# Optimization experiments

Hardware: AMD Instinct MI355X
Metric: run time of the kernel (lower is better)

## Reference

```python
import jax, jax.numpy as jnp
import numpy as np
from jax import lax

DN = ('NCHW', 'OIHW', 'NCHW')

def conv(x, w, b):
    y = lax.conv_general_dilated(x, w, (1, 1), 'SAME', dimension_numbers=DN)
    return y + b[None, :, None, None]


def setup_inputs() -> dict:
    key = jax.random.key(0)
    ks = jax.random.split(key, 32)
    B, C, H, W = 16, 256, 40, 100
    dim, N, kd, ncls, mdim = 134, 4, 128, 2, 256
    inc = C + 2
    s = 0.05  # weight init scale
    def w(k, shape):
        return jax.random.normal(k, shape, jnp.float32) * s
    d = {}
    d['features'] = jax.random.normal(ks[0], (B, C, H, W), jnp.float32)
    d['iw0'] = w(ks[1], (dim, inc, 3, 3)); d['ib0'] = jnp.zeros((dim,), jnp.float32)
    d['iw1'] = w(ks[2], (dim, dim, 3, 3)); d['ib1'] = jnp.zeros((dim,), jnp.float32)
    d['iw2'] = w(ks[3], (dim, dim, 3, 3)); d['ib2'] = jnp.zeros((dim,), jnp.float32)
    d['iw3'] = w(ks[4], (dim, dim, 3, 3)); d['ib3'] = jnp.zeros((dim,), jnp.float32)
    d['iam_w'] = w(ks[5], (N, dim, 3, 3)); d['iam_b'] = jnp.zeros((N,), jnp.float32)
    d['cls_w'] = w(ks[6], (ncls, dim));    d['cls_b'] = jnp.zeros((ncls,), jnp.float32)
    d['mk_w'] = w(ks[7], (kd, dim));       d['mk_b'] = jnp.zeros((kd,), jnp.float32)
    d['mw0'] = w(ks[8], (mdim, inc, 3, 3));  d['mb0'] = jnp.zeros((mdim,), jnp.float32)
    d['mw1'] = w(ks[9], (mdim, mdim, 3, 3)); d['mb1'] = jnp.zeros((mdim,), jnp.float32)
    d['mw2'] = w(ks[10], (mdim, mdim, 3, 3)); d['mb2'] = jnp.zeros((mdim,), jnp.float32)
    d['mw3'] = w(ks[11], (mdim, mdim, 3, 3)); d['mb3'] = jnp.zeros((mdim,), jnp.float32)
    d['pw'] = w(ks[12], (kd, mdim, 1, 1));   d['pb'] = jnp.zeros((kd,), jnp.float32)
    return d


def reference(features, iw0, ib0, iw1, ib1, iw2, ib2, iw3, ib3, iam_w, iam_b,
              cls_w, cls_b, mk_w, mk_b, mw0, mb0, mw1, mb1, mw2, mb2, mw3, mb3, pw, pb):
    B, C, H, W = features.shape
    # coordinate channels in [-1, 1]
    y_loc = -1.0 + 2.0 * jnp.arange(H, dtype=jnp.float32) / (H - 1)
    x_loc = -1.0 + 2.0 * jnp.arange(W, dtype=jnp.float32) / (W - 1)
    yy, xx = jnp.meshgrid(y_loc, x_loc, indexing='ij')  # [H,W]
    coords = jnp.broadcast_to(jnp.stack([xx, yy], 0)[None], (B, 2, H, W))
    feat = jnp.concatenate([coords, features], axis=1)  # [B, C+2, H, W]

    # instance branch conv stack (258 -> 134, relu)
    f = jax.nn.relu(conv(feat, iw0, ib0))
    f = jax.nn.relu(conv(f, iw1, ib1))
    f = jax.nn.relu(conv(f, iw2, ib2))
    f = jax.nn.relu(conv(f, iw3, ib3))  # [B,134,H,W]

    params = jnp.transpose(f, (0, 2, 3, 1)).reshape(-1, 134)  # [B*H*W, 134]

    iam = conv(f, iam_w, iam_b)           # [B,N,H,W]
    iam_prob = jax.nn.sigmoid(iam)
    Bn, Ni = iam_prob.shape[:2]

    # seed extraction: per-map flat argmax (pos = r*W + c, label always 0 in original)
    pos = jnp.argmax(iam_prob.reshape(Bn * Ni, H * W), axis=-1)  # [B*N], values in [0, H*W)
    sel = params[pos]                     # gather rows (indexes batch-0 region, as in source)
    mask_params = sel[:, :67]
    reg_params = sel[:, 67:]

    # iam-weighted pooling
    ip = iam_prob.reshape(Bn, Ni, H * W)
    ip = ip / jnp.clip(ip.sum(-1, keepdims=True), 1e-6)
    inst = jnp.einsum('bnl,bcl->bnc', ip, f.reshape(Bn, 134, H * W))  # [B,N,134]

    pred_logits = inst @ cls_w.T + cls_b  # [B,N,2]
    pred_kernel = inst @ mk_w.T + mk_b    # [B,N,128]

    # mask branch (258 -> 256 x4 relu, then 1x1 projection to 128, no relu)
    m = jax.nn.relu(conv(feat, mw0, mb0))
    m = jax.nn.relu(conv(m, mw1, mb1))
    m = jax.nn.relu(conv(m, mw2, mb2))
    m = jax.nn.relu(conv(m, mw3, mb3))
    mf = conv(m, pw, pb)                  # [B,128,H,W]

    pred_masks = jnp.einsum('bnk,bkl->bnl', pred_kernel, mf.reshape(Bn, 128, H * W))
    pred_masks = pred_masks.reshape(Bn * Ni, H, W)
    pred_logits = pred_logits.reshape(Bn * Ni, -1)
    return pred_logits, mask_params, reg_params, pred_masks
```

## Files before the change

### kernel.cpp

```cpp
#include <hip/hip_runtime.h>
#include <hip/hip_bf16.h>
#include <math.h>

constexpr int HW = 4000;
constexpr int HP = 4284;
constexpr int HPAD = 4480;
constexpr int NPIXH = 16 * HP;

typedef short s16x8 __attribute__((ext_vector_type(8)));
typedef float f32x4 __attribute__((ext_vector_type(4)));
typedef unsigned short u16x4 __attribute__((ext_vector_type(4)));
typedef unsigned short u16;

__device__ __forceinline__ u16 f2bf(float f) {
    __hip_bfloat16 h = __float2bfloat16(f);
    u16 b; __builtin_memcpy(&b, &h, 2); return b;
}
__device__ __forceinline__ float bf2f(u16 b) {
    __hip_bfloat16 h; __builtin_memcpy(&h, &b, 2); return __bfloat162float(h);
}

__device__ __forceinline__ void gload_lds16(const void* g, void* l) {
    __builtin_amdgcn_global_load_lds(
        (const __attribute__((address_space(1))) void*)g,
        (__attribute__((address_space(3))) void*)l, 16, 0, 0);
}

__global__ __launch_bounds__(256) void repack_w(
    const float* __restrict__ W, u16* __restrict__ Wh, u16* __restrict__ Wl,
    int Cout, int Cin, int NRS, int nCh, int Npad, int do_lo)
{
    const int chunk = blockIdx.x * 256 + threadIdx.x;
    const int per = Npad * 4;
    const int total = NRS * nCh * per;
    if (chunk >= total) return;
    const int q = chunk % per;
    const int t2 = chunk / per;
    const int ch = t2 % nCh;
    const int rs = t2 / nCh;
    const int f = q >> 6, g = (q >> 4) & 3, rA = q & 15;
    const int n = f * 16 + rA;
    u16x4 hp[2], lp[2];
    #pragma unroll
    for (int j = 0; j < 8; ++j) {
        const int c = ch * 32 + g * 8 + j;
        const float v = (n < Cout && c < Cin) ? W[((size_t)n * Cin + c) * NRS + rs] : 0.f;
        const u16 hb = f2bf(v);
        hp[j >> 2][j & 3] = hb;
        lp[j >> 2][j & 3] = f2bf(v - bf2f(hb));
    }
    const size_t o = (size_t)chunk * 8;
    *(u16x4*)(Wh + o) = hp[0]; *(u16x4*)(Wh + o + 4) = hp[1];
    if (do_lo) { *(u16x4*)(Wl + o) = lp[0]; *(u16x4*)(Wl + o + 4) = lp[1]; }
}

__global__ __launch_bounds__(256) void prep_x0(
    const float* __restrict__ feat, u16* __restrict__ Xh, u16* __restrict__ Xl)
{
    const int p = blockIdx.x * 256 + threadIdx.x;
    if (p >= NPIXH) return;
    const int b = p / HP; const int rem = p - b * HP;
    const int hh = rem / 102, wp = rem - hh * 102;
    const bool halo = (hh == 0) | (hh == 41) | (wp == 0) | (wp == 101);
    const int h = hh - 1, w = wp - 1;
    const int hw = h * 100 + w;
    const float xw = -1.f + 2.f * (float)w / 99.f;
    const float yh = -1.f + 2.f * (float)h / 39.f;
    for (int g = 0; g < 36; ++g) {
        u16x4 hp[2], lp[2];
        #pragma unroll
        for (int j = 0; j < 8; ++j) {
            const int c = g * 8 + j;
            float v = 0.f;
            if (!halo) {
                if (c == 0) v = xw;
                else if (c == 1) v = yh;
                else if (c < 258) v = feat[((size_t)(b * 256 + (c - 2))) * HW + hw];
            }
            const u16 hb = f2bf(v);
            hp[j >> 2][j & 3] = hb;
            lp[j >> 2][j & 3] = f2bf(v - bf2f(hb));
        }
        const size_t o = ((size_t)(b * 36 + g) * HPAD + rem) * 8;
        *(u16x4*)(Xh + o) = hp[0]; *(u16x4*)(Xh + o + 4) = hp[1];
        *(u16x4*)(Xl + o) = lp[0]; *(u16x4*)(Xl + o + 4) = lp[1];
    }
}

__global__ __launch_bounds__(256) void zero_halo_pl(
    u16* __restrict__ pa, u16* __restrict__ pb, int nGa, int nGb)
{
    const int p = blockIdx.x * 256 + threadIdx.x;
    if (p >= NPIXH) return;
    const int b = p / HP; const int rem = p - b * HP;
    const int hh = rem / 102, wp = rem - hh * 102;
    if (!((hh == 0) | (hh == 41) | (wp == 0) | (wp == 101))) return;
    const u16x4 z = {0, 0, 0, 0};
    for (int g = 0; g < nGa; ++g) {
        const size_t o = ((size_t)(b * nGa + g) * HPAD + rem) * 8;
        *(u16x4*)(pa + o) = z; *(u16x4*)(pa + o + 4) = z;
    }
    if (pb)
        for (int g = 0; g < nGb; ++g) {
            const size_t o = ((size_t)(b * nGb + g) * HPAD + rem) * 8;
            *(u16x4*)(pb + o) = z; *(u16x4*)(pb + o + 4) = z;
        }
}

template <int SPLIT, int BN, int NRS, int OUTMODE, int NCH>
__global__ __launch_bounds__(256, 2) void conv_mfma(
    const u16* __restrict__ Xhi, const u16* __restrict__ Xlo,
    const u16* __restrict__ Whi, const u16* __restrict__ Wlo,
    const float* __restrict__ bias,
    u16* __restrict__ Yhi, u16* __restrict__ Ylo, float* __restrict__ Yf,
    int Npad, int Cout, int CoutStore, int nGout, int do_relu,
    int nN, int cpx)
{
    constexpr int FW = BN / 32;
    constexpr int PSTRIDE = 393;
    constexpr int NGIN = NCH * 4;

    __shared__ u16 lsXh[4 * PSTRIDE * 8];
    __shared__ u16 lsXl[SPLIT == 3 ? 4 * PSTRIDE * 8 : 8];

    const int tid = threadIdx.x, lane = tid & 63, wid = tid >> 6;

    const int pb_ = blockIdx.x;
    const int s = (pb_ & 7) * cpx + (pb_ >> 3);
    const int nb = s % nN;
    const int mt = s / nN;
    const int mb = mt & 31, bimg = mt >> 5;
    const int off = mb * 128;
    const int n0 = nb * BN;
    const int h0 = off / 100, w0 = off - h0 * 100;
    const int pTL0 = h0 * 102 + w0;

    const int wn = (wid & 1) * (BN / 2);
    const int wm = (wid >> 1) * 64;
    const int gA = lane >> 4, rA = lane & 15;
    const int wq0 = ((n0 + wn) >> 4) * 64;

    int pd[4]; bool mval[4];
    #pragma unroll
    for (int fb = 0; fb < 4; ++fb) {
        int mm = off + wm + fb * 16 + rA;
        mval[fb] = mm < HW;
        if (!mval[fb]) mm = HW - 1;
        const int h = mm / 100, w = mm - h * 100;
        pd[fb] = (h * 102 + w) - pTL0;
    }

    auto stageX = [&](int ch) {
        const size_t src = ((size_t)(bimg * NGIN + ch * 4 + wid) * HPAD + pTL0) * 8;
        char* dst = (char*)lsXh + wid * (PSTRIDE * 16);
        char* dstl = (char*)lsXl + wid * (PSTRIDE * 16);
        #pragma unroll
        for (int i = 0; i < 6; ++i) {
            gload_lds16(Xhi + src + (size_t)(i * 64 + lane) * 8, dst + i * 1024);
            if constexpr (SPLIT == 3)
                gload_lds16(Xlo + src + (size_t)(i * 64 + lane) * 8, dstl + i * 1024);
        }
    };

    s16x8 wh[2][FW];
    s16x8 wl[2][SPLIT == 3 ? FW : 1];
    auto loadW = [&](int ch, int rs, int buf) {
        const size_t base = (((size_t)rs * NCH + ch) * (Npad * 4) + wq0 + lane) * 8;
        #pragma unroll
        for (int fa = 0; fa < FW; ++fa) {
            wh[buf][fa] = *(const s16x8*)(Whi + base + fa * 64 * 8);
            if constexpr (SPLIT == 3)
                wl[buf][fa] = *(const s16x8*)(Wlo + base + fa * 64 * 8);
        }
    };

    f32x4 acc[FW][4];
    #pragma unroll
    for (int i = 0; i < FW; ++i)
        #pragma unroll
        for (int j = 0; j < 4; ++j) acc[i][j] = (f32x4){0.f, 0.f, 0.f, 0.f};

    #pragma unroll 1
    for (int ch = 0; ch < NCH; ++ch) {
        if (ch) __syncthreads();
        stageX(ch);
        loadW(ch, 0, 0);
        __syncthreads();

        #pragma unroll
        for (int rs = 0; rs < NRS; ++rs) {
            if (rs + 1 < NRS) loadW(ch, rs + 1, (rs + 1) & 1);
            const int toff = (NRS == 9) ? ((rs / 3) * 102 + (rs % 3)) : 103;

            s16x8 bX[4], bXl[SPLIT == 3 ? 4 : 1];
            #pragma unroll
            for (int fb = 0; fb < 4; ++fb) {
                const int xi = (gA * PSTRIDE + pd[fb] + toff) * 8;
                bX[fb] = *(const s16x8*)&lsXh[xi];
                if constexpr (SPLIT == 3) bXl[fb] = *(const s16x8*)&lsXl[xi];
            }
            #pragma unroll
            for (int fa = 0; fa < FW; ++fa)
                #pragma unroll
                for (int fb = 0; fb < 4; ++fb) {
                    acc[fa][fb] = __builtin_amdgcn_mfma_f32_16x16x32_bf16(
                        wh[rs & 1][fa], bX[fb], acc[fa][fb], 0, 0, 0);
                    if constexpr (SPLIT == 3) {
                        acc[fa][fb] = __builtin_amdgcn_mfma_f32_16x16x32_bf16(
                            wh[rs & 1][fa], bXl[fb], acc[fa][fb], 0, 0, 0);
                        acc[fa][fb] = __builtin_amdgcn_mfma_f32_16x16x32_bf16(
                            wl[rs & 1][fa], bX[fb], acc[fa][fb], 0, 0, 0);
                    }
                }
        }
    }

    #pragma unroll
    for (int fb = 0; fb < 4; ++fb) {
        if (!mval[fb]) continue;
        const int mm = off + wm + fb * 16 + rA;
        #pragma unroll
        for (int fa = 0; fa < FW; ++fa) {
            const int nbc = n0 + wn + fa * 16 + gA * 4;
            if (nbc >= CoutStore) continue;
            f32x4 v = acc[fa][fb];
            #pragma unroll
            for (int i = 0; i < 4; ++i) {
                const int n = nbc + i;
                float x = (n < Cout) ? (v[i] + bias[n]) : 0.f;
                if (do_relu) x = fmaxf(x, 0.f);
                v[i] = x;
            }
            if constexpr (OUTMODE == 2) {
                *(f32x4*)(Yf + (size_t)(bimg * HW + mm) * CoutStore + nbc) = v;
            } else {
                const size_t o =
                    ((size_t)(bimg * nGout + (nbc >> 3)) * HPAD + pTL0 + pd[fb] + 103) * 8 + (nbc & 7);
                u16x4 hp;
                #pragma unroll
                for (int i = 0; i < 4; ++i) hp[i] = f2bf(v[i]);
                *(u16x4*)(Yhi + o) = hp;
                if constexpr (OUTMODE == 0) {
                    u16x4 lp;
                    #pragma unroll
                    for (int i = 0; i < 4; ++i) lp[i] = f2bf(v[i] - bf2f(hp[i]));
                    *(u16x4*)(Ylo + o) = lp;
                }
            }
        }
    }
}

__global__ __launch_bounds__(256) void iam_conv_nhwc(
    const u16* __restrict__ fhi, const u16* __restrict__ flo,
    const float* __restrict__ Wt, const float* __restrict__ bias,
    float* __restrict__ iam)
{
    __shared__ float wsm[9 * 134 * 4];
    const int tid = threadIdx.x;
    for (int i = tid; i < 4824; i += 256) {
        const int rs = i / 536; const int rem = i - rs * 536;
        const int c = rem >> 2; const int n = rem & 3;
        wsm[i] = Wt[(n * 134 + c) * 9 + rs];
    }
    __syncthreads();
    const int m = blockIdx.x * 256 + tid;
    const int b = m / HW; const int hw = m - b * HW;
    const int h = hw / 100, w = hw - h * 100;
    const int pTL = h * 102 + w;
    float a0 = bias[0], a1 = bias[1], a2 = bias[2], a3 = bias[3];
    for (int rs = 0; rs < 9; ++rs) {
        const int pA = pTL + (rs / 3) * 102 + (rs % 3);
        const float* wrow = &wsm[rs * 536];
        for (int g = 0; g < 17; ++g) {
            const size_t o = ((size_t)(b * 20 + g) * HPAD + pA) * 8;
            s16x8 hv = *(const s16x8*)(fhi + o);
            s16x8 lv = *(const s16x8*)(flo + o);
            #pragma unroll
            for (int j = 0; j < 8; ++j) {
                const int c = g * 8 + j;
                if (c < 134) {
                    const float v = bf2f((u16)hv[j]) + bf2f((u16)lv[j]);
                    const float* wc = wrow + c * 4;
                    a0 = fmaf(v, wc[0], a0); a1 = fmaf(v, wc[1], a1);
                    a2 = fmaf(v, wc[2], a2); a3 = fmaf(v, wc[3], a3);
                }
            }
        }
    }
    iam[(b * 4 + 0) * HW + hw] = a0;
    iam[(b * 4 + 1) * HW + hw] = a1;
    iam[(b * 4 + 2) * HW + hw] = a2;
    iam[(b * 4 + 3) * HW + hw] = a3;
}

__device__ __forceinline__ float sigmoidf_dev(float x) {
    return 1.f / (1.f + expf(-x));
}

__global__ __launch_bounds__(256) void stats_kernel(
    const float* __restrict__ iam, int* __restrict__ pos, float* __restrict__ denom)
{
    const int i = blockIdx.x;
    const int tid = threadIdx.x;
    const float* p = &iam[i * HW];
    float bm = -1e30f; int bi = 0; float sum = 0.f;
    for (int l = tid; l < HW; l += 256) {
        const float s = sigmoidf_dev(p[l]);
        sum += s;
        if (s > bm) { bm = s; bi = l; }
    }
    __shared__ float sm[256]; __shared__ int si[256]; __shared__ float ss[256];
    sm[tid] = bm; si[tid] = bi; ss[tid] = sum;
    __syncthreads();
    for (int off = 128; off > 0; off >>= 1) {
        if (tid < off) {
            ss[tid] += ss[tid + off];
            const float m2 = sm[tid + off]; const int i2 = si[tid + off];
            if (m2 > sm[tid] || (m2 == sm[tid] && i2 < si[tid])) { sm[tid] = m2; si[tid] = i2; }
        }
        __syncthreads();
    }
    if (tid == 0) { pos[i] = si[0]; denom[i] = fmaxf(ss[0], 1e-6f); }
}

__global__ __launch_bounds__(256) void inst_nhwc(
    const u16* __restrict__ fhi, const u16* __restrict__ flo,
    const float* __restrict__ iam, const float* __restrict__ denom,
    float* __restrict__ inst)
{
    const int b = blockIdx.x, g = blockIdx.y;
    const int tid = threadIdx.x;
    float acc[4][8] = {};
    const size_t pbase = (size_t)(b * 20 + g) * HPAD;
    for (int l = tid; l < HW; l += 256) {
        const int p = (l / 100 + 1) * 102 + (l % 100) + 1;
        s16x8 hv = *(const s16x8*)(fhi + (pbase + p) * 8);
        s16x8 lv = *(const s16x8*)(flo + (pbase + p) * 8);
        float fv[8];
        #pragma unroll
        for (int j = 0; j < 8; ++j) fv[j] = bf2f((u16)hv[j]) + bf2f((u16)lv[j]);
        #pragma unroll
        for (int n = 0; n < 4; ++n) {
            const float s = sigmoidf_dev(iam[(b * 4 + n) * HW + l]);
            #pragma unroll
            for (int j = 0; j < 8; ++j) acc[n][j] = fmaf(s, fv[j], acc[n][j]);
        }
    }
    __shared__ float red[128];
    const int lane = tid & 63, wid = tid >> 6;
    #pragma unroll
    for (int n = 0; n < 4; ++n)
        #pragma unroll
        for (int j = 0; j < 8; ++j) {
            float v = acc[n][j];
            #pragma unroll
            for (int off = 32; off > 0; off >>= 1) v += __shfl_xor(v, off);
            if (lane == 0) red[wid * 32 + n * 8 + j] = v;
        }
    __syncthreads();
    if (tid < 32) {
        const float s = red[tid] + red[32 + tid] + red[64 + tid] + red[96 + tid];
        const int n = tid >> 3, j = tid & 7;
        const int c = g * 8 + j;
        if (c < 134) inst[(b * 4 + n) * 134 + c] = s / denom[b * 4 + n];
    }
}

__global__ __launch_bounds__(128) void head_kernel(
    const float* __restrict__ inst,
    const float* __restrict__ cls_w, const float* __restrict__ cls_b,
    const float* __restrict__ mk_w, const float* __restrict__ mk_b,
    float* __restrict__ out_logits, float* __restrict__ pk)
{
    const int i = blockIdx.x;
    const int tid = threadIdx.x;
    __shared__ float iv[134];
    for (int c = tid; c < 134; c += 128) iv[c] = inst[i * 134 + c];
    __syncthreads();
    float a = mk_b[tid];
    for (int c = 0; c < 134; ++c) a = fmaf(iv[c], mk_w[tid * 134 + c], a);
    pk[i * 128 + tid] = a;
    if (tid < 2) {
        float g = cls_b[tid];
        for (int c = 0; c < 134; ++c) g = fmaf(iv[c], cls_w[tid * 134 + c], g);
        out_logits[i * 2 + tid] = g;
    }
}

__global__ void gather_nhwc(
    const u16* __restrict__ fhi, const u16* __restrict__ flo,
    const int* __restrict__ pos, float* __restrict__ outm, float* __restrict__ outr)
{
    const int i = blockIdx.x;
    const int c = threadIdx.x;
    if (c >= 134) return;
    const int p = pos[i];
    const int ph = (p / 100 + 1) * 102 + (p % 100) + 1;
    const size_t o = ((size_t)(c >> 3) * HPAD + ph) * 8 + (c & 7);
    const float v = bf2f(fhi[o]) + bf2f(flo[o]);
    if (c < 67) outm[i * 67 + c] = v;
    else        outr[i * 67 + (c - 67)] = v;
}

__global__ __launch_bounds__(256) void maskout_nhwc(
    const float* __restrict__ pk, const float* __restrict__ mf,
    float* __restrict__ outm)
{
    const int b = blockIdx.x, lc = blockIdx.y;
    const int tid = threadIdx.x;
    __shared__ float pks[4][128];
    for (int i = tid; i < 512; i += 256) pks[i >> 7][i & 127] = pk[b * 512 + i];
    __syncthreads();
    const int l = lc * 256 + tid;
    if (l >= HW) return;
    const float* row = mf + (size_t)(b * HW + l) * 128;
    float a[4] = {};
    for (int k = 0; k < 128; k += 4) {
        const f32x4 mv = *(const f32x4*)(row + k);
        #pragma unroll
        for (int n = 0; n < 4; ++n) {
            a[n] = fmaf(pks[n][k + 0], mv[0], a[n]);
            a[n] = fmaf(pks[n][k + 1], mv[1], a[n]);
            a[n] = fmaf(pks[n][k + 2], mv[2], a[n]);
            a[n] = fmaf(pks[n][k + 3], mv[3], a[n]);
        }
    }
    #pragma unroll
    for (int n = 0; n < 4; ++n) outm[(b * 4 + n) * HW + l] = a[n];
}

extern "C" void kernel_launch(void* const* d_in, const int* in_sizes, int n_in,
                              void* d_out, int out_size, void* d_ws, size_t ws_size,
                              hipStream_t stream)
{
    const float* features = (const float*)d_in[0];
    const float* iw0 = (const float*)d_in[1];
    const float* ib0 = (const float*)d_in[2];
    const float* iw1 = (const float*)d_in[3];
    const float* ib1 = (const float*)d_in[4];
    const float* iw2 = (const float*)d_in[5];
    const float* ib2 = (const float*)d_in[6];
    const float* iw3 = (const float*)d_in[7];
    const float* ib3 = (const float*)d_in[8];
    const float* iam_w = (const float*)d_in[9];
    const float* iam_b = (const float*)d_in[10];
    const float* cls_w = (const float*)d_in[11];
    const float* cls_b = (const float*)d_in[12];
    const float* mk_w = (const float*)d_in[13];
    const float* mk_b = (const float*)d_in[14];
    const float* mw0 = (const float*)d_in[15];
    const float* mb0 = (const float*)d_in[16];
    const float* mw1 = (const float*)d_in[17];
    const float* mb1 = (const float*)d_in[18];
    const float* mw2 = (const float*)d_in[19];
    const float* mb2 = (const float*)d_in[20];
    const float* mw3 = (const float*)d_in[21];
    const float* mb3 = (const float*)d_in[22];
    const float* pw = (const float*)d_in[23];
    const float* pb = (const float*)d_in[24];

    constexpr size_t WI0 = (size_t)9 * 9 * 160 * 4 * 16;
    constexpr size_t WI123 = (size_t)9 * 5 * 160 * 4 * 16;
    constexpr size_t WM0 = (size_t)9 * 9 * 256 * 4 * 16;
    constexpr size_t WM123 = (size_t)9 * 8 * 256 * 4 * 16;
    constexpr size_t WPJ = (size_t)1 * 8 * 128 * 4 * 16;
    constexpr size_t PLANE = (size_t)HPAD * 16;
    constexpr size_t X0SZ = (size_t)16 * 36 * PLANE;
    constexpr size_t P20 = (size_t)16 * 20 * PLANE;

    char* ws = (char*)d_ws;
    size_t off = 0;
    auto carve = [&](size_t bytes) { char* p = ws + off; off += (bytes + 255) & ~(size_t)255; return p; };
    u16* wi0h = (u16*)carve(WI0); u16* wi0l = (u16*)carve(WI0);
    u16* wi1h = (u16*)carve(WI123); u16* wi1l = (u16*)carve(WI123);
    u16* wi2h = (u16*)carve(WI123); u16* wi2l = (u16*)carve(WI123);
    u16* wi3h = (u16*)carve(WI123); u16* wi3l = (u16*)carve(WI123);
    u16* wm0h = (u16*)carve(WM0);
    u16* wm1h = (u16*)carve(WM123); u16* wm2h = (u16*)carve(WM123); u16* wm3h = (u16*)carve(WM123);
    u16* wpjh = (u16*)carve(WPJ);
    u16* X0hi = (u16*)carve(X0SZ);
    char* RGA = carve(X0SZ);
    char* RGB = carve(2 * P20);
    char* RGC = carve(2 * P20);
    float* iamb = (float*)carve(1024000);
    int* pos = (int*)carve(256);
    float* denom = (float*)carve(256);
    float* instb = (float*)carve(34560);
    float* pkbuf = (float*)carve(32768);

    u16* X0lo = (u16*)RGA;
    u16* MBhi = (u16*)RGA;
    u16* RAhi = (u16*)RGB; u16* RAlo = (u16*)(RGB + P20);
    u16* MAhi = (u16*)RGB;
    u16* RBhi = (u16*)RGC; u16* RBlo = (u16*)(RGC + P20);
    float* mf = (float*)RGC;

    float* out_logits = (float*)d_out;
    float* out_mask = out_logits + 128;
    float* out_reg = out_mask + 64 * 67;
    float* out_masks = out_reg + 64 * 67;

    const dim3 blk(256);
    auto rp = [&](const float* W, u16* h, u16* l, int Cout_, int Cin_, int NRS_,
                  int nCh_, int Npad_, int dolo) {
        const int tot = NRS_ * nCh_ * Npad_ * 4;
        repack_w<<<dim3((tot + 255) / 256), blk, 0, stream>>>(W, h, l, Cout_, Cin_, NRS_, nCh_, Npad_, dolo);
    };
    rp(iw0, wi0h, wi0l, 134, 258, 9, 9, 160, 1);
    rp(iw1, wi1h, wi1l, 134, 134, 9, 5, 160, 1);
    rp(iw2, wi2h, wi2l, 134, 134, 9, 5, 160, 1);
    rp(iw3, wi3h, wi3l, 134, 134, 9, 5, 160, 1);
    rp(mw0, wm0h, nullptr, 256, 258, 9, 9, 256, 0);
    rp(mw1, wm1h, nullptr, 256, 256, 9, 8, 256, 0);
    rp(mw2, wm2h, nullptr, 256, 256, 9, 8, 256, 0);
    rp(mw3, wm3h, nullptr, 256, 256, 9, 8, 256, 0);
    rp(pw, wpjh, nullptr, 128, 256, 1, 8, 128, 0);

    const dim3 gH((NPIXH + 255) / 256);
    prep_x0<<<gH, blk, 0, stream>>>(features, X0hi, X0lo);
    zero_halo_pl<<<gH, blk, 0, stream>>>(RAhi, RAlo, 20, 20);

    conv_mfma<3, 160, 9, 0, 9><<<dim3(512), blk, 0, stream>>>(
        X0hi, X0lo, wi0h, wi0l, ib0, RAhi, RAlo, nullptr, 160, 134, 160, 20, 1, 1, 64);
    zero_halo_pl<<<gH, blk, 0, stream>>>(RBhi, RBlo, 20, 20);
    conv_mfma<3, 160, 9, 0, 5><<<dim3(512), blk, 0, stream>>>(
        RAhi, RAlo, wi1h, wi1l, ib1, RBhi, RBlo, nullptr, 160, 134, 160, 20, 1, 1, 64);
    conv_mfma<3, 160, 9, 0, 5><<<dim3(512), blk, 0, stream>>>(
        RBhi, RBlo, wi2h, wi2l, ib2, RAhi, RAlo, nullptr, 160, 134, 160, 20, 1, 1, 64);
    conv_mfma<3, 160, 9, 0, 5><<<dim3(512), blk, 0, stream>>>(
        RAhi, RAlo, wi3h, wi3l, ib3, RBhi, RBlo, nullptr, 160, 134, 160, 20, 1, 1, 64);

    iam_conv_nhwc<<<dim3(250), blk, 0, stream>>>(RBhi, RBlo, iam_w, iam_b, iamb);
    stats_kernel<<<dim3(64), blk, 0, stream>>>(iamb, pos, denom);
    inst_nhwc<<<dim3(16, 17), blk, 0, stream>>>(RBhi, RBlo, iamb, denom, instb);
    head_kernel<<<dim3(64), dim3(128), 0, stream>>>(instb, cls_w, cls_b, mk_w, mk_b, out_logits, pkbuf);
    gather_nhwc<<<dim3(64), dim3(192), 0, stream>>>(RBhi, RBlo, pos, out_mask, out_reg);

    zero_halo_pl<<<gH, blk, 0, stream>>>(MAhi, MBhi, 32, 32);
    conv_mfma<1, 256, 9, 1, 9><<<dim3(512), blk, 0, stream>>>(
        X0hi, nullptr, wm0h, nullptr, mb0, MAhi, nullptr, nullptr, 256, 256, 256, 32, 1, 1, 64);
    conv_mfma<1, 256, 9, 1, 8><<<dim3(512), blk, 0, stream>>>(
        MAhi, nullptr, wm1h, nullptr, mb1, MBhi, nullptr, nullptr, 256, 256, 256, 32, 1, 1, 64);
    conv_mfma<1, 256, 9, 1, 8><<<dim3(512), blk, 0, stream>>>(
        MBhi, nullptr, wm2h, nullptr, mb2, MAhi, nullptr, nullptr, 256, 256, 256, 32, 1, 1, 64);
    conv_mfma<1, 256, 9, 1, 8><<<dim3(512), blk, 0, stream>>>(
        MAhi, nullptr, wm3h, nullptr, mb3, MBhi, nullptr, nullptr, 256, 256, 256, 32, 1, 1, 64);
    conv_mfma<1, 128, 1, 2, 8><<<dim3(512), blk, 0, stream>>>(
        MBhi, nullptr, wpjh, nullptr, pb, nullptr, nullptr, mf, 128, 128, 128, 0, 0, 1, 64);

    maskout_nhwc<<<dim3(16, 16), blk, 0, stream>>>(pkbuf, mf, out_masks);
}
```

Before: 1.248 ms.

## Split conv N-tiles smaller, two-pass hi/lo staging, raise occupancy

The conv kernel now stages the hi and lo input planes in two sequential passes through a single LDS buffer, halving shared memory per block. The instance branch switches from BN=160 to BN=64 with 3 N-blocks and 1536 blocks at min 4 waves per EU, and the mask branch from BN=256 to BN=128 with 1024 blocks at min 3. The aim is more resident blocks and fewer registers per wave, to hide latency and balance the grid. In exchange, each input tile and weight tile is loaded more often, and the split-bf16 path restages the input twice per channel chunk.

After: 1.125 ms. -9.9%, faster.

```diff
diff --git a/kernel.cpp b/kernel.cpp
--- a/kernel.cpp
+++ b/kernel.cpp
@@ -107,8 +107,8 @@
         }
 }
 
-template <int SPLIT, int BN, int NRS, int OUTMODE, int NCH>
-__global__ __launch_bounds__(256, 2) void conv_mfma(
+template <int SPLIT, int BN, int NRS, int OUTMODE, int NCH, int MINW>
+__global__ __launch_bounds__(256, MINW) void conv_mfma(
     const u16* __restrict__ Xhi, const u16* __restrict__ Xlo,
     const u16* __restrict__ Whi, const u16* __restrict__ Wlo,
     const float* __restrict__ bias,
@@ -119,9 +119,9 @@
     constexpr int FW = BN / 32;
     constexpr int PSTRIDE = 393;
     constexpr int NGIN = NCH * 4;
-
-    __shared__ u16 lsXh[4 * PSTRIDE * 8];
-    __shared__ u16 lsXl[SPLIT == 3 ? 4 * PSTRIDE * 8 : 8];
+    constexpr int NPASS = (SPLIT == 3) ? 2 : 1;
+
+    __shared__ u16 lsX[4 * PSTRIDE * 8];
 
     const int tid = threadIdx.x, lane = tid & 63, wid = tid >> 6;
 
@@ -150,29 +150,16 @@
         pd[fb] = (h * 102 + w) - pTL0;
     }
 
-    auto stageX = [&](int ch) {
+    auto stageX = [&](const u16* __restrict__ Xsrc, int ch) {
         const size_t src = ((size_t)(bimg * NGIN + ch * 4 + wid) * HPAD + pTL0) * 8;
-        char* dst = (char*)lsXh + wid * (PSTRIDE * 16);
-        char* dstl = (char*)lsXl + wid * (PSTRIDE * 16);
-        #pragma unroll
-        for (int i = 0; i < 6; ++i) {
-            gload_lds16(Xhi + src + (size_t)(i * 64 + lane) * 8, dst + i * 1024);
-            if constexpr (SPLIT == 3)
-                gload_lds16(Xlo + src + (size_t)(i * 64 + lane) * 8, dstl + i * 1024);
-        }
+        char* dst = (char*)lsX + wid * (PSTRIDE * 16);
+        #pragma unroll
+        for (int i = 0; i < 6; ++i)
+            gload_lds16(Xsrc + src + (size_t)(i * 64 + lane) * 8, dst + i * 1024);
     };
 
     s16x8 wh[2][FW];
     s16x8 wl[2][SPLIT == 3 ? FW : 1];
-    auto loadW = [&](int ch, int rs, int buf) {
-        const size_t base = (((size_t)rs * NCH + ch) * (Npad * 4) + wq0 + lane) * 8;
-        #pragma unroll
-        for (int fa = 0; fa < FW; ++fa) {
-            wh[buf][fa] = *(const s16x8*)(Whi + base + fa * 64 * 8);
-            if constexpr (SPLIT == 3)
-                wl[buf][fa] = *(const s16x8*)(Wlo + base + fa * 64 * 8);
-        }
-    };
 
     f32x4 acc[FW][4];
     #pragma unroll
@@ -180,38 +167,55 @@
         #pragma unroll
         for (int j = 0; j < 4; ++j) acc[i][j] = (f32x4){0.f, 0.f, 0.f, 0.f};
 
-    #pragma unroll 1
-    for (int ch = 0; ch < NCH; ++ch) {
-        if (ch) __syncthreads();
-        stageX(ch);
-        loadW(ch, 0, 0);
-        __syncthreads();
-
-        #pragma unroll
-        for (int rs = 0; rs < NRS; ++rs) {
-            if (rs + 1 < NRS) loadW(ch, rs + 1, (rs + 1) & 1);
-            const int toff = (NRS == 9) ? ((rs / 3) * 102 + (rs % 3)) : 103;
-
-            s16x8 bX[4], bXl[SPLIT == 3 ? 4 : 1];
+    #pragma unroll
+    for (int pass = 0; pass < NPASS; ++pass) {
+        const u16* Xsrc = (NPASS == 2 && pass == 1) ? Xlo : Xhi;
+        constexpr bool HASLO = (SPLIT == 3);
+        const bool withLo = HASLO && (pass == 0);
+
+        auto loadW = [&](int ch, int rs, int buf) {
+            const size_t base = (((size_t)rs * NCH + ch) * (Npad * 4) + wq0 + lane) * 8;
             #pragma unroll
-            for (int fb = 0; fb < 4; ++fb) {
-                const int xi = (gA * PSTRIDE + pd[fb] + toff) * 8;
-                bX[fb] = *(const s16x8*)&lsXh[xi];
-                if constexpr (SPLIT == 3) bXl[fb] = *(const s16x8*)&lsXl[xi];
+            for (int fa = 0; fa < FW; ++fa) {
+                wh[buf][fa] = *(const s16x8*)(Whi + base + fa * 64 * 8);
+                if constexpr (HASLO) {
+                    if (withLo)
+                        wl[buf][fa] = *(const s16x8*)(Wlo + base + fa * 64 * 8);
+                }
             }
+        };
+
+        #pragma unroll 1
+        for (int ch = 0; ch < NCH; ++ch) {
+            if (ch | pass) __syncthreads();
+            stageX(Xsrc, ch);
+            loadW(ch, 0, 0);
+            __syncthreads();
+
             #pragma unroll
-            for (int fa = 0; fa < FW; ++fa)
+            for (int rs = 0; rs < NRS; ++rs) {
+                if (rs + 1 < NRS) loadW(ch, rs + 1, (rs + 1) & 1);
+                const int toff = (NRS == 9) ? ((rs / 3) * 102 + (rs % 3)) : 103;
+
+                s16x8 bX[4];
                 #pragma unroll
                 for (int fb = 0; fb < 4; ++fb) {
-                    acc[fa][fb] = __builtin_amdgcn_mfma_f32_16x16x32_bf16(
-                        wh[rs & 1][fa], bX[fb], acc[fa][fb], 0, 0, 0);
-                    if constexpr (SPLIT == 3) {
+                    const int xi = (gA * PSTRIDE + pd[fb] + toff) * 8;
+                    bX[fb] = *(const s16x8*)&lsX[xi];
+                }
+                #pragma unroll
+                for (int fa = 0; fa < FW; ++fa)
+                    #pragma unroll
+                    for (int fb = 0; fb < 4; ++fb) {
                         acc[fa][fb] = __builtin_amdgcn_mfma_f32_16x16x32_bf16(
-                            wh[rs & 1][fa], bXl[fb], acc[fa][fb], 0, 0, 0);
-                        acc[fa][fb] = __builtin_amdgcn_mfma_f32_16x16x32_bf16(
-                            wl[rs & 1][fa], bX[fb], acc[fa][fb], 0, 0, 0);
+                            wh[rs & 1][fa], bX[fb], acc[fa][fb], 0, 0, 0);
+                        if constexpr (HASLO) {
+                            if (pass == 0)
+                                acc[fa][fb] = __builtin_amdgcn_mfma_f32_16x16x32_bf16(
+                                    wl[rs & 1][fa], bX[fb], acc[fa][fb], 0, 0, 0);
+                        }
                     }
-                }
+            }
         }
     }
 
@@ -521,15 +525,15 @@
     prep_x0<<<gH, blk, 0, stream>>>(features, X0hi, X0lo);
     zero_halo_pl<<<gH, blk, 0, stream>>>(RAhi, RAlo, 20, 20);
 
-    conv_mfma<3, 160, 9, 0, 9><<<dim3(512), blk, 0, stream>>>(
-        X0hi, X0lo, wi0h, wi0l, ib0, RAhi, RAlo, nullptr, 160, 134, 160, 20, 1, 1, 64);
+    conv_mfma<3, 64, 9, 0, 9, 4><<<dim3(1536), blk, 0, stream>>>(
+        X0hi, X0lo, wi0h, wi0l, ib0, RAhi, RAlo, nullptr, 160, 134, 160, 20, 1, 3, 192);
     zero_halo_pl<<<gH, blk, 0, stream>>>(RBhi, RBlo, 20, 20);
-    conv_mfma<3, 160, 9, 0, 5><<<dim3(512), blk, 0, stream>>>(
-        RAhi, RAlo, wi1h, wi1l, ib1, RBhi, RBlo, nullptr, 160, 134, 160, 20, 1, 1, 64);
-    conv_mfma<3, 160, 9, 0, 5><<<dim3(512), blk, 0, stream>>>(
-        RBhi, RBlo, wi2h, wi2l, ib2, RAhi, RAlo, nullptr, 160, 134, 160, 20, 1, 1, 64);
-    conv_mfma<3, 160, 9, 0, 5><<<dim3(512), blk, 0, stream>>>(
-        RAhi, RAlo, wi3h, wi3l, ib3, RBhi, RBlo, nullptr, 160, 134, 160, 20, 1, 1, 64);
+    conv_mfma<3, 64, 9, 0, 5, 4><<<dim3(1536), blk, 0, stream>>>(
+        RAhi, RAlo, wi1h, wi1l, ib1, RBhi, RBlo, nullptr, 160, 134, 160, 20, 1, 3, 192);
+    conv_mfma<3, 64, 9, 0, 5, 4><<<dim3(1536), blk, 0, stream>>>(
+        RBhi, RBlo, wi2h, wi2l, ib2, RAhi, RAlo, nullptr, 160, 134, 160, 20, 1, 3, 192);
+    conv_mfma<3, 64, 9, 0, 5, 4><<<dim3(1536), blk, 0, stream>>>(
+        RAhi, RAlo, wi3h, wi3l, ib3, RBhi, RBlo, nullptr, 160, 134, 160, 20, 1, 3, 192);
 
     iam_conv_nhwc<<<dim3(250), blk, 0, stream>>>(RBhi, RBlo, iam_w, iam_b, iamb);
     stats_kernel<<<dim3(64), blk, 0, stream>>>(iamb, pos, denom);
@@ -538,15 +542,15 @@
     gather_nhwc<<<dim3(64), dim3(192), 0, stream>>>(RBhi, RBlo, pos, out_mask, out_reg);
 
     zero_halo_pl<<<gH, blk, 0, stream>>>(MAhi, MBhi, 32, 32);
-    conv_mfma<1, 256, 9, 1, 9><<<dim3(512), blk, 0, stream>>>(
-        X0hi, nullptr, wm0h, nullptr, mb0, MAhi, nullptr, nullptr, 256, 256, 256, 32, 1, 1, 64);
-    conv_mfma<1, 256, 9, 1, 8><<<dim3(512), blk, 0, stream>>>(
-        MAhi, nullptr, wm1h, nullptr, mb1, MBhi, nullptr, nullptr, 256, 256, 256, 32, 1, 1, 64);
-    conv_mfma<1, 256, 9, 1, 8><<<dim3(512), blk, 0, stream>>>(
-        MBhi, nullptr, wm2h, nullptr, mb2, MAhi, nullptr, nullptr, 256, 256, 256, 32, 1, 1, 64);
-    conv_mfma<1, 256, 9, 1, 8><<<dim3(512), blk, 0, stream>>>(
-        MAhi, nullptr, wm3h, nullptr, mb3, MBhi, nullptr, nullptr, 256, 256, 256, 32, 1, 1, 64);
-    conv_mfma<1, 128, 1, 2, 8><<<dim3(512), blk, 0, stream>>>(
+    conv_mfma<1, 128, 9, 1, 9, 3><<<dim3(1024), blk, 0, stream>>>(
+        X0hi, nullptr, wm0h, nullptr, mb0, MAhi, nullptr, nullptr, 256, 256, 256, 32, 1, 2, 128);
+    conv_mfma<1, 128, 9, 1, 8, 3><<<dim3(1024), blk, 0, stream>>>(
+        MAhi, nullptr, wm1h, nullptr, mb1, MBhi, nullptr, nullptr, 256, 256, 256, 32, 1, 2, 128);
+    conv_mfma<1, 128, 9, 1, 8, 3><<<dim3(1024), blk, 0, stream>>>(
+        MBhi, nullptr, wm2h, nullptr, mb2, MAhi, nullptr, nullptr, 256, 256, 256, 32, 1, 2, 128);
+    conv_mfma<1, 128, 9, 1, 8, 3><<<dim3(1024), blk, 0, stream>>>(
+        MAhi, nullptr, wm3h, nullptr, mb3, MBhi, nullptr, nullptr, 256, 256, 256, 32, 1, 2, 128);
+    conv_mfma<1, 128, 1, 2, 8, 3><<<dim3(512), blk, 0, stream>>>(
         MBhi, nullptr, wpjh, nullptr, pb, nullptr, nullptr, mf, 128, 128, 128, 0, 0, 1, 64);
 
     maskout_nhwc<<<dim3(16, 16), blk, 0, stream>>>(pkbuf, mf, out_masks);
```
